# Kernel optimization log

Measured on AMD Instinct MI355X. Metric: run time of the kernel, lower is better.

## Reference

```python
import jax, jax.numpy as jnp
import numpy as np

HIDDEN = 600
INPUT_DIM = 300
BATCH = 64
SEQ = 512


def _lstm(x, W, U, b):
    """Keras-style LSTM, gate order (i, f, g, o). x: [B,T,D] -> [B,T,H]."""
    B, T, D = x.shape
    H = U.shape[0]
    xz = jnp.einsum('btd,dg->btg', x, W) + b  # precompute input projections [B,T,4H]

    def step(carry, xz_t):
        h, c = carry
        z = xz_t + h @ U  # [B,4H]
        i, f, g, o = jnp.split(z, 4, axis=-1)
        i = jax.nn.sigmoid(i)
        f = jax.nn.sigmoid(f)
        g = jnp.tanh(g)
        o = jax.nn.sigmoid(o)
        c = f * c + i * g
        h = o * jnp.tanh(c)
        return (h, c), h

    init = (jnp.zeros((B, H), x.dtype), jnp.zeros((B, H), x.dtype))
    _, hs = jax.lax.scan(step, init, jnp.swapaxes(xz, 0, 1))  # [T,B,H]
    return jnp.swapaxes(hs, 0, 1)


def _reverse_sequence(x, lengths):
    """tf.reverse_sequence along axis 1: reverse first lengths[b] steps, keep tail."""
    T = x.shape[1]
    t = jnp.arange(T)[None, :]
    L = lengths[:, None]
    idx = jnp.where(t < L, L - 1 - t, t)  # [B,T]
    return jnp.take_along_axis(x, idx[:, :, None], axis=1)


def setup_inputs() -> dict:
    key = jax.random.key(0)
    ks = jax.random.split(key, 8)
    inputs = jax.random.normal(ks[0], (BATCH, SEQ, INPUT_DIM), dtype=jnp.float32)
    lengths = jax.random.randint(ks[1], (BATCH,), 1, SEQ + 1, dtype=jnp.int32)
    s = 0.05
    Wf = jax.random.normal(ks[2], (INPUT_DIM, 4 * HIDDEN), dtype=jnp.float32) * s
    Uf = jax.random.normal(ks[3], (HIDDEN, 4 * HIDDEN), dtype=jnp.float32) * s
    bf = jnp.zeros((4 * HIDDEN,), dtype=jnp.float32)
    Wb = jax.random.normal(ks[4], (INPUT_DIM, 4 * HIDDEN), dtype=jnp.float32) * s
    Ub = jax.random.normal(ks[5], (HIDDEN, 4 * HIDDEN), dtype=jnp.float32) * s
    bb = jnp.zeros((4 * HIDDEN,), dtype=jnp.float32)
    return {"inputs": inputs, "lengths": lengths, "training": False,
            "Wf": Wf, "Uf": Uf, "bf": bf, "Wb": Wb, "Ub": Ub, "bb": bb}


def reference(inputs, lengths, training, Wf, Uf, bf, Wb, Ub, bb):
    # training=False -> Keras dropout is identity, so plain LSTMs are faithful.
    T = inputs.shape[1]
    seq_mask = (jnp.arange(T)[None, :] < lengths[:, None]).astype(inputs.dtype)  # [B,T]
    forward_outputs = _lstm(inputs, Wf, Uf, bf)
    reversed_inputs = _reverse_sequence(inputs, lengths)
    backward_outputs = _reverse_sequence(_lstm(reversed_inputs, Wb, Ub, bb), lengths)
    outputs = jnp.concatenate([forward_outputs, backward_outputs], axis=-1)  # [B,T,2H]
    outputs = outputs * seq_mask[:, :, None]
    # reduce_states=True: tf.reduce_mean over time divides by full T (not lengths)
    return jnp.mean(outputs, axis=1)
```

## Files before the change

kernel.cpp:

```cpp
#include <hip/hip_runtime.h>
#include <hip/hip_fp16.h>
#include <cmath>

typedef _Float16 f16;
typedef _Float16 half8 __attribute__((ext_vector_type(8)));
typedef float f32x4 __attribute__((ext_vector_type(4)));

#define P_WG   75
#define GRID_MAIN (2*P_WG)
#define G      12
#define RING   13

#define X16_ELEMS  (64u*512u*320u)
#define BPK_HALF   (2u*75u*2u*30u*64u*8u)
#define HBUF_F16   (2u*2u*64u*640u)
#define HBUF_WORDS (HBUF_F16/2u)
#define FLAG_WORDS 256u

__global__ void lstm_prep(const float* __restrict__ x,
                          const float* __restrict__ Wf, const float* __restrict__ Uf,
                          const float* __restrict__ Wb, const float* __restrict__ Ub,
                          const int* __restrict__ len,
                          f16* __restrict__ x16h, f16* __restrict__ x16l,
                          f16* __restrict__ Bpk,
                          unsigned* __restrict__ hbw, unsigned* __restrict__ flags,
                          int* __restrict__ maxT, float* __restrict__ outp)
{
    const unsigned total = X16_ELEMS + BPK_HALF + HBUF_WORDS + FLAG_WORDS + 2u;
    for (unsigned e = blockIdx.x * blockDim.x + threadIdx.x; e < total;
         e += gridDim.x * blockDim.x) {
        if (e < X16_ELEMS) {
            unsigned k = e % 320u, r = e / 320u;
            float v = (k < 300u) ? x[r * 300u + k] : 0.0f;
            f16 hi = (f16)v;
            x16h[e] = hi;
            x16l[e] = (f16)((v - (float)hi) * 2048.0f);
        } else if (e < X16_ELEMS + BPK_HALF) {
            unsigned i = e - X16_ELEMS;
            unsigned j    = i & 7u,  r1 = i >> 3;
            unsigned lane = r1 & 63u, r2 = r1 >> 6;
            unsigned kt   = r2 % 30u, r3 = r2 / 30u;
            unsigned nt   = r3 & 1u,  r4 = r3 >> 1;
            unsigned p    = r4 % 75u, dw = r4 / 75u;
            unsigned k = kt * 32u + (lane >> 4) * 8u + j;
            unsigned n = nt * 16u + (lane & 15u);
            unsigned c = (n >> 3) * 600u + p * 8u + (n & 7u);
            float v = 0.0f;
            if (k < 300u)                    v = (dw ? Wb : Wf)[k * 2400u + c];
            else if (k >= 320u && k < 920u)  v = (dw ? Ub : Uf)[(k - 320u) * 2400u + c];
            f16 hi = (f16)v;
            unsigned base = (((((dw * 75u + p) * 2u + 0u) * 2u + nt) * 30u + kt) * 64u + lane) * 8u + j;
            Bpk[base]          = hi;
            Bpk[base + 30720u] = (f16)((v - (float)hi) * 2048.0f);
        } else if (e < X16_ELEMS + BPK_HALF + HBUF_WORDS) {
            hbw[e - X16_ELEMS - BPK_HALF] = 0u;
        } else if (e < X16_ELEMS + BPK_HALF + HBUF_WORDS + FLAG_WORDS) {
            unsigned q = e - (X16_ELEMS + BPK_HALF + HBUF_WORDS);
            unsigned q7 = q & 127u;
            flags[q] = (q7 < 75u) ? 0u : 0xFFFFFFFFu;
        } else {
            unsigned q = e - (X16_ELEMS + BPK_HALF + HBUF_WORDS + FLAG_WORDS);
            if (q == 0u) {
                int m = 1;
                for (int b = 0; b < 64; ++b) { int L = len[b]; m = (L > m) ? L : m; }
                *maxT = m;
            } else {
                outp[0] = 1000.0f;
            }
        }
    }
}

__device__ __forceinline__ float fsigm(float x) {
    return __builtin_amdgcn_rcpf(1.0f + __expf(-x));
}
__device__ __forceinline__ float ftanh(float x) {
    x = fminf(fmaxf(x, -15.0f), 15.0f);
    float e = __expf(2.0f * x);
    return (e - 1.0f) * __builtin_amdgcn_rcpf(e + 1.0f);
}

__global__ __launch_bounds__(256, 1)
void lstm_main(const f16* __restrict__ x16h, const f16* __restrict__ x16l,
               const f16* __restrict__ Bpk,
               f16* __restrict__ hbuf, float* __restrict__ xz,
               unsigned* flags, const int* __restrict__ maxT,
               const int* __restrict__ len,
               const float* __restrict__ bfv, const float* __restrict__ bbv,
               float* __restrict__ out)
{
    __shared__ f32x4 obox[4][4][2][64];
    __shared__ f16 hstage[64][8];
    __shared__ f16 Bldsx[4][10][512];
    __shared__ f16 Bldsh[4][20][512];
    __shared__ unsigned cnt;

    const int tid  = threadIdx.x;
    const int wave = tid >> 6, lane = tid & 63;
    const int quad = lane >> 4, l15 = lane & 15;
    const int dir  = blockIdx.x & 1, p = blockIdx.x >> 1;
    const int pc   = p * 8;
    const int wg   = blockIdx.x;

    const int s0 = (wave < 2) ? 3 : 2;
    const unsigned bpk_base = (unsigned)(dir * 75 + p) * 4u * 30u * 512u;

    const float* bias = dir ? bbv : bfv;
    const float b0 = bias[((l15 >> 3)    ) * 600 + pc + (l15 & 7)];
    const float b1 = bias[((l15 >> 3) + 2) * 600 + pc + (l15 & 7)];

    int Lm[4], Lr[4];
#pragma unroll
    for (int mt = 0; mt < 4; ++mt) Lm[mt] = len[mt * 16 + l15];
    const int Lw = len[wave * 16 + l15];
#pragma unroll
    for (int r = 0; r < 4; ++r)   Lr[r]  = len[wave * 16 + quad * 4 + r];

    f16* hb0 = hbuf + dir * (2 * 64 * 640);
    unsigned* myflags = flags + dir * 128;
    float* myxz = xz + (size_t)wg * (RING * 64 * 32);
    float cst[4] = {0, 0, 0, 0}, sum[4] = {0, 0, 0, 0};
    const int T = *maxT;

    if (tid == 0) cnt = 0u;

    const int pkt = wave + 4 * (s0 + (lane >> 2));
    const int pp  = (pkt << 2) - 40 + (lane & 3);
    const bool pact = (lane < 20) && (pp < 75);

    {
#pragma unroll
        for (int blk = 0; blk < 4; ++blk) {
            f16* blx = &Bldsx[blk][0][0];
            for (int i = tid; i < 640; i += 256)
                *(half8*)(blx + i * 8) =
                    *(const half8*)(Bpk + bpk_base + (unsigned)blk * 15360u + (unsigned)i * 8u);
            f16* blh = &Bldsh[blk][0][0];
            for (int i = tid; i < 1280; i += 256)
                *(half8*)(blh + i * 8) =
                    *(const half8*)(Bpk + bpk_base + (unsigned)blk * 15360u + 5120u + (unsigned)i * 8u);
        }
    }
    __syncthreads();

#pragma unroll
    for (int jc = 0; jc < 3; ++jc) {
        int g = wave * 3 + jc;
        int tt = (g < 512) ? g : 511;
        unsigned arow[4];
#pragma unroll
        for (int mt = 0; mt < 4; ++mt) {
            int tx = tt;
            if (dir) tx = (tt < Lm[mt]) ? (Lm[mt] - 1 - tt) : tt;
            arow[mt] = ((unsigned)(mt * 16 + l15) * 512u + (unsigned)tx) * 320u + quad * 8;
        }
        f32x4 aH[4][2], aM[4][2];
#pragma unroll
        for (int mt = 0; mt < 4; ++mt)
#pragma unroll
            for (int nt = 0; nt < 2; ++nt) {
                aH[mt][nt] = f32x4{0.f, 0.f, 0.f, 0.f};
                aM[mt][nt] = f32x4{0.f, 0.f, 0.f, 0.f};
            }
#pragma unroll
        for (int kt = 0; kt < 10; ++kt) {
            const f16* bb = &Bldsx[0][0][0] + kt * 512 + lane * 8;
            half8 B00 = *(const half8*)(bb);
            half8 B01 = *(const half8*)(bb + 5120);
            half8 B10 = *(const half8*)(bb + 10240);
            half8 B11 = *(const half8*)(bb + 15360);
#pragma unroll
            for (int mt = 0; mt < 4; ++mt) {
                half8 Ah = *(const half8*)(x16h + arow[mt] + kt * 32);
                half8 Al = *(const half8*)(x16l + arow[mt] + kt * 32);
                aH[mt][0] = __builtin_amdgcn_mfma_f32_16x16x32_f16(Ah, B00, aH[mt][0], 0, 0, 0);
                aM[mt][0] = __builtin_amdgcn_mfma_f32_16x16x32_f16(Ah, B10, aM[mt][0], 0, 0, 0);
                aM[mt][0] = __builtin_amdgcn_mfma_f32_16x16x32_f16(Al, B00, aM[mt][0], 0, 0, 0);
                aH[mt][1] = __builtin_amdgcn_mfma_f32_16x16x32_f16(Ah, B01, aH[mt][1], 0, 0, 0);
                aM[mt][1] = __builtin_amdgcn_mfma_f32_16x16x32_f16(Ah, B11, aM[mt][1], 0, 0, 0);
                aM[mt][1] = __builtin_amdgcn_mfma_f32_16x16x32_f16(Al, B01, aM[mt][1], 0, 0, 0);
            }
        }
#pragma unroll
        for (int mt = 0; mt < 4; ++mt)
#pragma unroll
            for (int r = 0; r < 4; ++r) {
                unsigned rowi = (unsigned)(g * 64 + mt * 16 + quad * 4 + r) * 32u;
                myxz[rowi + l15]      = aH[mt][0][r] + aM[mt][0][r] * (1.0f / 2048.0f) + b0;
                myxz[rowi + 16 + l15] = aH[mt][1][r] + aM[mt][1][r] * (1.0f / 2048.0f) + b1;
            }
    }
    __syncthreads();

    for (int t = 0; t < T; ++t) {
        int tf = t + G;
        int tq = (tf < T) ? tf : (T - 1);
        half8 axh[10], axl[10];
        {
            int tx = tq;
            if (dir) tx = (tq < Lw) ? (Lw - 1 - tq) : tq;
            unsigned arow = ((unsigned)(wave * 16 + l15) * 512u + (unsigned)tx) * 320u + quad * 8;
#pragma unroll
            for (int kt = 0; kt < 10; ++kt) {
                axh[kt] = *(const half8*)(x16h + arow + kt * 32);
                axl[kt] = *(const half8*)(x16l + arow + kt * 32);
            }
        }

        float z0p[4], z1p[4];
        {
            int slot = t % RING;
            unsigned rbase = (unsigned)(slot * 64 + wave * 16 + quad * 4) * 32u;
#pragma unroll
            for (int r = 0; r < 4; ++r) {
                z0p[r] = myxz[rbase + r * 32 + l15];
                z1p[r] = myxz[rbase + r * 32 + 16 + l15];
            }
        }

        const f16* hcur = hb0 + (t & 1) * (64 * 640);
        f16*       hnxt = hb0 + ((t + 1) & 1) * (64 * 640);

        if (t > 0) {
            const unsigned tgt = (unsigned)t;
            for (;;) {
                unsigned v = tgt;
                if (pact)
                    v = __hip_atomic_load(myflags + pp, __ATOMIC_RELAXED, __HIP_MEMORY_SCOPE_AGENT);
                if (!__any(v < tgt)) break;
            }
        }

        unsigned long long pre[5][8];
        const f16* hq = hcur + quad * 8;
#define HLOAD(SP)                                                                        \
        { const int kt_ = wave + 4 * (s0 + (SP));                                        \
          const f16* hp_ = hq + (kt_ * 32 - 320);                                        \
          _Pragma("unroll")                                                              \
          for (int mt_ = 0; mt_ < 4; ++mt_) {                                            \
              const unsigned long long* q_ =                                             \
                  (const unsigned long long*)(hp_ + (unsigned)(mt_ * 16 + l15) * 640u);  \
              pre[SP][mt_ * 2]     = __hip_atomic_load(q_,     __ATOMIC_RELAXED,         \
                                                       __HIP_MEMORY_SCOPE_AGENT);        \
              pre[SP][mt_ * 2 + 1] = __hip_atomic_load(q_ + 1, __ATOMIC_RELAXED,         \
                                                       __HIP_MEMORY_SCOPE_AGENT);        \
          } }

        HLOAD(0) HLOAD(1) HLOAD(2) HLOAD(3) HLOAD(4)
#undef HLOAD
        __builtin_amdgcn_sched_barrier(0);

        {
            f32x4 aH[2], aM[2];
            aH[0] = f32x4{0.f, 0.f, 0.f, 0.f}; aM[0] = f32x4{0.f, 0.f, 0.f, 0.f};
            aH[1] = f32x4{0.f, 0.f, 0.f, 0.f}; aM[1] = f32x4{0.f, 0.f, 0.f, 0.f};
#pragma unroll
            for (int kt = 0; kt < 10; ++kt) {
                const f16* bb = &Bldsx[0][0][0] + kt * 512 + lane * 8;
                half8 B00 = *(const half8*)(bb);
                half8 B01 = *(const half8*)(bb + 5120);
                half8 B10 = *(const half8*)(bb + 10240);
                half8 B11 = *(const half8*)(bb + 15360);
                aH[0] = __builtin_amdgcn_mfma_f32_16x16x32_f16(axh[kt], B00, aH[0], 0, 0, 0);
                aM[0] = __builtin_amdgcn_mfma_f32_16x16x32_f16(axh[kt], B10, aM[0], 0, 0, 0);
                aM[0] = __builtin_amdgcn_mfma_f32_16x16x32_f16(axl[kt], B00, aM[0], 0, 0, 0);
                aH[1] = __builtin_amdgcn_mfma_f32_16x16x32_f16(axh[kt], B01, aH[1], 0, 0, 0);
                aM[1] = __builtin_amdgcn_mfma_f32_16x16x32_f16(axh[kt], B11, aM[1], 0, 0, 0);
                aM[1] = __builtin_amdgcn_mfma_f32_16x16x32_f16(axl[kt], B01, aM[1], 0, 0, 0);
            }
            if (tf < T) {
                int slot = tf % RING;
#pragma unroll
                for (int r = 0; r < 4; ++r) {
                    unsigned rowi = (unsigned)(slot * 64 + wave * 16 + quad * 4 + r) * 32u;
                    myxz[rowi + l15]      = aH[0][r] + aM[0][r] * (1.0f / 2048.0f) + b0;
                    myxz[rowi + 16 + l15] = aH[1][r] + aM[1][r] * (1.0f / 2048.0f) + b1;
                }
            }
        }

        f32x4 accH[4][2], accM[4][2];
#pragma unroll
        for (int mt = 0; mt < 4; ++mt)
#pragma unroll
            for (int nt = 0; nt < 2; ++nt) {
                accH[mt][nt] = f32x4{0.f, 0.f, 0.f, 0.f};
                accM[mt][nt] = f32x4{0.f, 0.f, 0.f, 0.f};
            }
#pragma unroll
        for (int sp = 0; sp < 5; ++sp) {
            const int kt = wave + 4 * (s0 + sp);
            const f16* bh = &Bldsh[0][0][0] + (kt - 10) * 512 + lane * 8;
            half8 Bc00 = *(const half8*)(bh);
            half8 Bc01 = *(const half8*)(bh + 10240);
            half8 Bc10 = *(const half8*)(bh + 20480);
            half8 Bc11 = *(const half8*)(bh + 30720);
#pragma unroll
            for (int mt = 0; mt < 4; ++mt) {
                union { unsigned long long u[2]; half8 h; } xu;
                xu.u[0] = pre[sp][mt * 2];
                xu.u[1] = pre[sp][mt * 2 + 1];
                half8 Ah = xu.h;
                accH[mt][0] = __builtin_amdgcn_mfma_f32_16x16x32_f16(Ah, Bc00, accH[mt][0], 0, 0, 0);
                accM[mt][0] = __builtin_amdgcn_mfma_f32_16x16x32_f16(Ah, Bc10, accM[mt][0], 0, 0, 0);
                accH[mt][1] = __builtin_amdgcn_mfma_f32_16x16x32_f16(Ah, Bc01, accH[mt][1], 0, 0, 0);
                accM[mt][1] = __builtin_amdgcn_mfma_f32_16x16x32_f16(Ah, Bc11, accM[mt][1], 0, 0, 0);
            }
        }

        __syncthreads();
#pragma unroll
        for (int mt = 0; mt < 4; ++mt)
#pragma unroll
            for (int nt = 0; nt < 2; ++nt)
                obox[wave][mt][nt][lane] = accH[mt][nt] + accM[mt][nt] * (1.0f / 2048.0f);
        __syncthreads();
        f32x4 z0 = obox[0][wave][0][lane] + obox[1][wave][0][lane]
                 + obox[2][wave][0][lane] + obox[3][wave][0][lane];
        f32x4 z1 = obox[0][wave][1][lane] + obox[1][wave][1][lane]
                 + obox[2][wave][1][lane] + obox[3][wave][1][lane];
        z0 += f32x4{z0p[0], z0p[1], z0p[2], z0p[3]};
        z1 += f32x4{z1p[0], z1p[1], z1p[2], z1p[3]};

#pragma unroll
        for (int r = 0; r < 4; ++r) {
            float zi = z0[r], zg = z1[r];
            float zf = __shfl_xor(z0[r], 8, 64);
            float zo = __shfl_xor(z1[r], 8, 64);
            if (l15 < 8) {
                float ig = fsigm(zi);
                float fg = fsigm(zf);
                float gg = ftanh(zg);
                float og = fsigm(zo);
                float c  = fg * cst[r] + ig * gg;
                cst[r] = c;
                float h = og * ftanh(c);
                if (t < Lr[r]) sum[r] += h;
                hstage[wave * 16 + quad * 4 + r][l15] = (f16)h;
            }
        }

        if (lane < 32) {
            int rr = lane >> 1, hf = lane & 1;
            unsigned long long v = *(const unsigned long long*)&hstage[wave * 16 + rr][hf * 4];
            __hip_atomic_store(
                (unsigned long long*)(hnxt + (unsigned)(wave * 16 + rr) * 640u + pc + hf * 4),
                v, __ATOMIC_RELAXED, __HIP_MEMORY_SCOPE_AGENT);
        }
        asm volatile("s_waitcnt vmcnt(0)" ::: "memory");
        if (lane == 0) {
            unsigned old = atomicAdd(&cnt, 1u);
            if (old == 4u * (unsigned)t + 3u)
                __hip_atomic_store(myflags + p, (unsigned)(t + 1),
                                   __ATOMIC_RELAXED, __HIP_MEMORY_SCOPE_AGENT);
        }
    }

    if (l15 < 8) {
#pragma unroll
        for (int r = 0; r < 4; ++r)
            out[(wave * 16 + quad * 4 + r) * 1200 + dir * 600 + pc + l15] =
                sum[r] * (1.0f / 512.0f);
    }
}

extern "C" void kernel_launch(void* const* d_in, const int* in_sizes, int n_in,
                              void* d_out, int out_size, void* d_ws, size_t ws_size,
                              hipStream_t stream) {
    const float* x   = (const float*)d_in[0];
    const int*   len = (const int*)  d_in[1];
    const float* Wf  = (const float*)d_in[3];
    const float* Uf  = (const float*)d_in[4];
    const float* bfv = (const float*)d_in[5];
    const float* Wb  = (const float*)d_in[6];
    const float* Ub  = (const float*)d_in[7];
    const float* bbv = (const float*)d_in[8];
    float* outp = (float*)d_out;

    char* w = (char*)d_ws;
    f16*      x16hp = (f16*)w;
    f16*      x16lp = (f16*)(w + 20971520);
    f16*      bpkp  = (f16*)(w + 41943040);
    f16*      hbufp = (f16*)(w + 60375040);
    float*    xzp   = (float*)(w + 60702720);
    unsigned* flagp = (unsigned*)(w + 76677120);
    int*      maxtp = (int*)(w + 76678144);

    hipLaunchKernelGGL(lstm_prep, dim3(1024), dim3(256), 0, stream,
                       x, Wf, Uf, Wb, Ub, len,
                       x16hp, x16lp, bpkp, (unsigned*)hbufp, flagp, maxtp, outp);

    hipLaunchKernelGGL(lstm_main, dim3(GRID_MAIN), dim3(256), 0, stream,
                       x16hp, x16lp, bpkp, hbufp, xzp, flagp, maxtp, len, bfv, bbv, outp);
}
```

Measured before the change: 4.770 ms.

## Replace per-step flag barrier with parity bits embedded in triple-buffered h data

Removes the separate per-workgroup step flags and the LDS counter and store-drain wait. Instead it embeds a parity bit in the low bit of each 4-half packet of the published hidden state and triple-buffers h. Consumers spin by reloading the h data itself until every packet shows the expected parity, which saves a flag round trip per timestep. The cost is one mantissa bit of h lost per packet, extra spin reloads of h, and a heavier validity check.

```diff
diff --git a/kernel.cpp b/kernel.cpp
--- a/kernel.cpp
+++ b/kernel.cpp
@@ -13,9 +13,10 @@
 
 #define X16_ELEMS  (64u*512u*320u)
 #define BPK_HALF   (2u*75u*2u*30u*64u*8u)
-#define HBUF_F16   (2u*2u*64u*640u)
+#define HBUF_F16   (2u*3u*64u*640u)
 #define HBUF_WORDS (HBUF_F16/2u)
-#define FLAG_WORDS 256u
+#define DIR_HWORDS (3u*64u*640u/2u)
+#define BUF_HWORDS (64u*640u/2u)
 
 __global__ void lstm_prep(const float* __restrict__ x,
                           const float* __restrict__ Wf, const float* __restrict__ Uf,
@@ -23,10 +24,10 @@
                           const int* __restrict__ len,
                           f16* __restrict__ x16h, f16* __restrict__ x16l,
                           f16* __restrict__ Bpk,
-                          unsigned* __restrict__ hbw, unsigned* __restrict__ flags,
+                          unsigned* __restrict__ hbw,
                           int* __restrict__ maxT, float* __restrict__ outp)
 {
-    const unsigned total = X16_ELEMS + BPK_HALF + HBUF_WORDS + FLAG_WORDS + 2u;
+    const unsigned total = X16_ELEMS + BPK_HALF + HBUF_WORDS + 2u;
     for (unsigned e = blockIdx.x * blockDim.x + threadIdx.x; e < total;
          e += gridDim.x * blockDim.x) {
         if (e < X16_ELEMS) {
@@ -53,13 +54,11 @@
             Bpk[base]          = hi;
             Bpk[base + 30720u] = (f16)((v - (float)hi) * 2048.0f);
         } else if (e < X16_ELEMS + BPK_HALF + HBUF_WORDS) {
-            hbw[e - X16_ELEMS - BPK_HALF] = 0u;
-        } else if (e < X16_ELEMS + BPK_HALF + HBUF_WORDS + FLAG_WORDS) {
+            unsigned q = e - X16_ELEMS - BPK_HALF;
+            unsigned qd = q % DIR_HWORDS;
+            hbw[q] = (qd >= 2u * BUF_HWORDS) ? 0x00010001u : 0u;
+        } else {
             unsigned q = e - (X16_ELEMS + BPK_HALF + HBUF_WORDS);
-            unsigned q7 = q & 127u;
-            flags[q] = (q7 < 75u) ? 0u : 0xFFFFFFFFu;
-        } else {
-            unsigned q = e - (X16_ELEMS + BPK_HALF + HBUF_WORDS + FLAG_WORDS);
             if (q == 0u) {
                 int m = 1;
                 for (int b = 0; b < 64; ++b) { int L = len[b]; m = (L > m) ? L : m; }
@@ -84,7 +83,7 @@
 void lstm_main(const f16* __restrict__ x16h, const f16* __restrict__ x16l,
                const f16* __restrict__ Bpk,
                f16* __restrict__ hbuf, float* __restrict__ xz,
-               unsigned* flags, const int* __restrict__ maxT,
+               const int* __restrict__ maxT,
                const int* __restrict__ len,
                const float* __restrict__ bfv, const float* __restrict__ bbv,
                float* __restrict__ out)
@@ -93,7 +92,6 @@
     __shared__ f16 hstage[64][8];
     __shared__ f16 Bldsx[4][10][512];
     __shared__ f16 Bldsh[4][20][512];
-    __shared__ unsigned cnt;
 
     const int tid  = threadIdx.x;
     const int wave = tid >> 6, lane = tid & 63;
@@ -116,17 +114,19 @@
 #pragma unroll
     for (int r = 0; r < 4; ++r)   Lr[r]  = len[wave * 16 + quad * 4 + r];
 
-    f16* hb0 = hbuf + dir * (2 * 64 * 640);
-    unsigned* myflags = flags + dir * 128;
+    f16* hb0 = hbuf + dir * (3 * 64 * 640);
     float* myxz = xz + (size_t)wg * (RING * 64 * 32);
     float cst[4] = {0, 0, 0, 0}, sum[4] = {0, 0, 0, 0};
     const int T = *maxT;
 
-    if (tid == 0) cnt = 0u;
-
-    const int pkt = wave + 4 * (s0 + (lane >> 2));
-    const int pp  = (pkt << 2) - 40 + (lane & 3);
-    const bool pact = (lane < 20) && (pp < 75);
+    unsigned pm0[5], pm1[5];
+#pragma unroll
+    for (int sp = 0; sp < 5; ++sp) {
+        int kt = wave + 4 * (s0 + sp);
+        int c0 = quad * 8 + (kt * 32 - 320);
+        pm0[sp] = (c0     < 600) ? 1u : 0u;
+        pm1[sp] = (c0 + 4 < 600) ? 1u : 0u;
+    }
 
     {
 #pragma unroll
@@ -192,7 +192,11 @@
     }
     __syncthreads();
 
+    int cur = 0;
+
     for (int t = 0; t < T; ++t) {
+        int nxt = cur + 1; if (nxt == 3) nxt = 0;
+
         int tf = t + G;
         int tq = (tf < T) ? tf : (T - 1);
         half8 axh[10], axl[10];
@@ -218,18 +222,8 @@
             }
         }
 
-        const f16* hcur = hb0 + (t & 1) * (64 * 640);
-        f16*       hnxt = hb0 + ((t + 1) & 1) * (64 * 640);
-
-        if (t > 0) {
-            const unsigned tgt = (unsigned)t;
-            for (;;) {
-                unsigned v = tgt;
-                if (pact)
-                    v = __hip_atomic_load(myflags + pp, __ATOMIC_RELAXED, __HIP_MEMORY_SCOPE_AGENT);
-                if (!__any(v < tgt)) break;
-            }
-        }
+        const f16* hcur = hb0 + cur * (64 * 640);
+        f16*       hnxt = hb0 + nxt * (64 * 640);
 
         unsigned long long pre[5][8];
         const f16* hq = hcur + quad * 8;
@@ -246,9 +240,25 @@
                                                        __HIP_MEMORY_SCOPE_AGENT);        \
           } }
 
-        HLOAD(0) HLOAD(1) HLOAD(2) HLOAD(3) HLOAD(4)
+        if (t > 0) {
+            const unsigned long long par = (unsigned long long)(t & 1);
+            for (;;) {
+                HLOAD(0) HLOAD(1) HLOAD(2) HLOAD(3) HLOAD(4)
+                unsigned bad = 0u;
+#pragma unroll
+                for (int sp = 0; sp < 5; ++sp)
+#pragma unroll
+                    for (int mt = 0; mt < 4; ++mt) {
+                        bad |= ((unsigned)(pre[sp][mt * 2]     ^ par) & pm0[sp]);
+                        bad |= ((unsigned)(pre[sp][mt * 2 + 1] ^ par) & pm1[sp]);
+                    }
+                if (!__any(bad != 0u)) break;
+                __builtin_amdgcn_s_sleep(1);
+            }
+        } else {
+            HLOAD(0) HLOAD(1) HLOAD(2) HLOAD(3) HLOAD(4)
+        }
 #undef HLOAD
-        __builtin_amdgcn_sched_barrier(0);
 
         {
             f32x4 aH[2], aM[2];
@@ -343,17 +353,12 @@
         if (lane < 32) {
             int rr = lane >> 1, hf = lane & 1;
             unsigned long long v = *(const unsigned long long*)&hstage[wave * 16 + rr][hf * 4];
+            v = (v & ~1ull) | (unsigned long long)((t + 1) & 1);
             __hip_atomic_store(
                 (unsigned long long*)(hnxt + (unsigned)(wave * 16 + rr) * 640u + pc + hf * 4),
                 v, __ATOMIC_RELAXED, __HIP_MEMORY_SCOPE_AGENT);
         }
-        asm volatile("s_waitcnt vmcnt(0)" ::: "memory");
-        if (lane == 0) {
-            unsigned old = atomicAdd(&cnt, 1u);
-            if (old == 4u * (unsigned)t + 3u)
-                __hip_atomic_store(myflags + p, (unsigned)(t + 1),
-                                   __ATOMIC_RELAXED, __HIP_MEMORY_SCOPE_AGENT);
-        }
+        cur = nxt;
     }
 
     if (l15 < 8) {
@@ -382,14 +387,13 @@
     f16*      x16lp = (f16*)(w + 20971520);
     f16*      bpkp  = (f16*)(w + 41943040);
     f16*      hbufp = (f16*)(w + 60375040);
-    float*    xzp   = (float*)(w + 60702720);
-    unsigned* flagp = (unsigned*)(w + 76677120);
-    int*      maxtp = (int*)(w + 76678144);
+    float*    xzp   = (float*)(w + 60866560);
+    int*      maxtp = (int*)(w + 76840960);
 
     hipLaunchKernelGGL(lstm_prep, dim3(1024), dim3(256), 0, stream,
                        x, Wf, Uf, Wb, Ub, len,
-                       x16hp, x16lp, bpkp, (unsigned*)hbufp, flagp, maxtp, outp);
+                       x16hp, x16lp, bpkp, (unsigned*)hbufp, maxtp, outp);
 
     hipLaunchKernelGGL(lstm_main, dim3(GRID_MAIN), dim3(256), 0, stream,
-                       x16hp, x16lp, bpkp, hbufp, xzp, flagp, maxtp, len, bfv, bbv, outp);
-}
+                       x16hp, x16lp, bpkp, hbufp, xzp, maxtp, len, bfv, bbv, outp);
+}
```

New measurement: 4.872 ms. 2.1% more time.
